# Optimization experiments

Measured on AMD Instinct MI355X. Metric: run time of the kernel, lower is better.

The kernel has to match this reference:

```python
import jax, jax.numpy as jnp
import numpy as np

BATCH, NODE, DIM = 4, 2048, 128
EPS = 1e-5


def _bn(x, gamma, beta):
    # BatchNorm1d in training mode: biased batch stats over rows, per-feature.
    mu = jnp.mean(x, axis=0)
    var = jnp.var(x, axis=0)
    return (x - mu) * jax.lax.rsqrt(var + EPS) * gamma + beta


def setup_inputs() -> dict:
    key = jax.random.key(0)
    ks = jax.random.split(key, 8)
    N = BATCH * NODE
    # Scale L like a normalized graph operator so activations stay sane.
    L = jax.random.normal(ks[0], (N, N), dtype=jnp.float32) / np.sqrt(N)
    inputs = jax.random.normal(ks[1], (BATCH, NODE, DIM), dtype=jnp.float32)
    mask = jnp.zeros((BATCH, NODE, 1), dtype=bool)  # unused in forward
    lim = 1.0 / np.sqrt(2 * DIM)
    fc0_w = jax.random.uniform(ks[2], (DIM, 2 * DIM), jnp.float32, -lim, lim)
    fc0_b = jax.random.uniform(ks[3], (DIM,), jnp.float32, -lim, lim)
    fc1_w = jax.random.uniform(ks[4], (DIM, 2 * DIM), jnp.float32, -lim, lim)
    fc1_b = jax.random.uniform(ks[5], (DIM,), jnp.float32, -lim, lim)
    bn0_gamma = jnp.ones((2 * DIM,), jnp.float32)
    bn0_beta = jnp.zeros((2 * DIM,), jnp.float32)
    bn1_gamma = jnp.ones((2 * DIM,), jnp.float32)
    bn1_beta = jnp.zeros((2 * DIM,), jnp.float32)
    return dict(L=L, mask=mask, inputs=inputs,
                bn0_gamma=bn0_gamma, bn0_beta=bn0_beta, fc0_w=fc0_w, fc0_b=fc0_b,
                bn1_gamma=bn1_gamma, bn1_beta=bn1_beta, fc1_w=fc1_w, fc1_b=fc1_b)


def reference(L, mask, inputs, bn0_gamma, bn0_beta, fc0_w, fc0_b,
              bn1_gamma, bn1_beta, fc1_w, fc1_b):
    b, n, d = inputs.shape

    def block(x, gamma, beta, w, bias):
        # x: (b, n, d). Laplacian propagation over flattened batch*node dim.
        xf = x.reshape(-1, d)                      # (b*n, d)
        Lx = (L @ xf).reshape(b, n, d)
        h = jnp.concatenate([x, Lx], axis=2).reshape(-1, 2 * d)
        h = _bn(h, gamma, beta)                    # pre-BN
        h = h @ w.T + bias                         # Linear(2d -> d)
        return h.reshape(b, n, d)

    x = jax.nn.elu(inputs)
    x = block(x, bn0_gamma, bn0_beta, fc0_w, fc0_b)
    x = jax.nn.elu(x)
    x = block(x, bn1_gamma, bn1_beta, fc1_w, fc1_b)
    return x + inputs
```

## Files before the change

### kernel.cpp

```cpp
#include <hip/hip_runtime.h>
#include <math.h>

#define NROWS 8192
#define DIM   128
#define FEAT  256
#define BK    128
#define NT    (NROWS / BK)

typedef __attribute__((ext_vector_type(8))) __bf16 bf16x8;
typedef __attribute__((ext_vector_type(8))) unsigned short u16x8;
typedef __attribute__((ext_vector_type(4))) unsigned short u16x4;
typedef __attribute__((ext_vector_type(4))) float f32x4;

__device__ __forceinline__ float bf2f(unsigned short h) {
  return __uint_as_float(((unsigned)h) << 16);
}
__device__ __forceinline__ unsigned short f2bf(float f) {
  unsigned u = __float_as_uint(f);
  return (unsigned short)((u + 0x7fff + ((u >> 16) & 1)) >> 16);
}
__device__ __forceinline__ void async16(const void* g, void* l) {
  __builtin_amdgcn_global_load_lds(
      (const __attribute__((address_space(1))) void*)g,
      (__attribute__((address_space(3))) void*)l, 16, 0, 0);
}
__device__ __forceinline__ f32x4 mfma16(bf16x8 a, bf16x8 b, f32x4 c) {
  return __builtin_amdgcn_mfma_f32_16x16x32_bf16(a, b, c, 0, 0, 0);
}
__device__ __forceinline__ float ldp(const void* p, int i, int is32) {
  return is32 ? ((const float*)p)[i] : bf2f(((const unsigned short*)p)[i]);
}

__global__ void detect_kernel(const unsigned short* __restrict__ L,
                              int* __restrict__ flag,
                              float* __restrict__ stats)
{
  for (int i = threadIdx.x; i < 1024; i += 256) stats[i] = 0.f;
  __shared__ int cnt;
  if (threadIdx.x == 0) cnt = 0;
  __syncthreads();
  int c = 0;
  for (int i = 0; i < 16; i++) {
    unsigned short s = L[2 * (threadIdx.x + 256 * i)];
    int e = (s >> 7) & 0xFF;
    if (e >= 192) c++;
  }
  atomicAdd(&cnt, c);
  __syncthreads();
  if (threadIdx.x == 0) *flag = (cnt > 16) ? 1 : 0;
}

__global__ __launch_bounds__(256) void trans_kernel(
    const void* __restrict__ src, unsigned short* __restrict__ xT,
    unsigned short* __restrict__ x0, unsigned short* __restrict__ inpc,
    float* __restrict__ stats, const int* __restrict__ flag)
{
  __shared__ __align__(16) unsigned short T[128 * 136];
  const int tid = threadIdx.x;
  const int r0 = blockIdx.x * 128;
  const int is32 = *flag;
  #pragma unroll
  for (int i = 0; i < 8; i++) {
    const int c = tid + 256 * i;
    const int rr = c >> 4, cg = c & 15;
    const size_t gidx = (size_t)(r0 + rr) * DIM + cg * 8;
    u16x8 v;
    if (is32) {
      const float* s = (const float*)src + gidx;
      f32x4 a = *(const f32x4*)s, b = *(const f32x4*)(s + 4);
      #pragma unroll
      for (int e = 0; e < 4; e++) { v[e] = f2bf(a[e]); v[e + 4] = f2bf(b[e]); }
    } else {
      v = *(const u16x8*)((const unsigned short*)src + gidx);
    }
    *(u16x8*)(inpc + gidx) = v;
    #pragma unroll
    for (int e = 0; e < 8; e++) {
      float f = bf2f(v[e]);
      f = f > 0.f ? f : expm1f(f);
      v[e] = f2bf(f);
    }
    *(u16x8*)(x0 + gidx) = v;
    *(u16x8*)(T + rr * 136 + cg * 8) = v;
  }
  __syncthreads();
  #pragma unroll
  for (int i = 0; i < 8; i++) {
    const int c = tid + 256 * i;
    const int n = c >> 4, mg = c & 15;
    u16x8 v;
    float s = 0.f, q = 0.f;
    #pragma unroll
    for (int e = 0; e < 8; e++) {
      unsigned short h = T[(mg * 8 + e) * 136 + n];
      v[e] = h;
      float f = bf2f(h);
      s += f; q += f * f;
    }
    *(u16x8*)(xT + (size_t)n * NROWS + r0 + mg * 8) = v;
    #pragma unroll
    for (int off = 1; off < 16; off <<= 1) {
      s += __shfl_xor(s, off, 16);
      q += __shfl_xor(q, off, 16);
    }
    if ((tid & 15) == 0) {
      atomicAdd(&stats[n], s);
      atomicAdd(&stats[256 + n], q);
    }
  }
}

template <int IS32>
__device__ __forceinline__ void gemm1_body(
    const void* __restrict__ Lraw, const unsigned short* __restrict__ xT,
    unsigned short* __restrict__ Lxb, float* __restrict__ stats,
    unsigned short* __restrict__ AsBase, unsigned short* __restrict__ BsBase)
{
  const int tid  = threadIdx.x;
  const int lane = tid & 63;
  const int wave = tid >> 6;
  const int wm = wave >> 2, wn = wave & 3;
  const int ln = lane & 15, quad = lane >> 4;
  const int m0 = blockIdx.x * 32;

  const int arow = tid >> 4, ap = tid & 15;
  const int akg = (ap & 8) | ((ap & 7) ^ (arow & 7));
  const float*          Lf = (const float*)Lraw;
  const unsigned short* Lh = (const unsigned short*)Lraw;
  const size_t Abase = (size_t)(m0 + arow) * NROWS + akg * 8;

  int brow[4], bkg[4];
  #pragma unroll
  for (int i = 0; i < 4; i++) {
    const int c = tid + (i << 9);
    brow[i] = c >> 4;
    const int p = c & 15;
    bkg[i] = (p & 8) | ((p & 7) ^ (brow[i] & 7));
  }

  unsigned short* a0 = AsBase;
  unsigned short* a1 = AsBase + 32 * 128;
  unsigned short* a2 = AsBase + 2 * 32 * 128;
  unsigned short* c0 = BsBase;
  unsigned short* c1 = BsBase + 128 * 128;
  unsigned short* c2 = BsBase + 2 * 128 * 128;

  f32x4 acc[2];
  acc[0] = (f32x4){0.f, 0.f, 0.f, 0.f};
  acc[1] = (f32x4){0.f, 0.f, 0.f, 0.f};

  auto issueB = [&](int kt, unsigned short* Bbuf) {
    const size_t koff = (size_t)kt * BK;
    #pragma unroll
    for (int i = 0; i < 4; i++) {
      const int c = tid + (i << 9);
      async16(xT + (size_t)brow[i] * NROWS + koff + bkg[i] * 8, Bbuf + c * 8);
    }
  };
  auto loadA = [&](int kt, f32x4& r0, f32x4& r1) {
    const float* s = Lf + Abase + (size_t)kt * BK;
    r0 = *(const f32x4*)s;
    r1 = *(const f32x4*)(s + 4);
  };
  auto issueA16 = [&](int kt, unsigned short* Abuf) {
    async16(Lh + Abase + (size_t)kt * BK, Abuf + arow * 128 + ap * 8);
  };
  auto writeA = [&](const f32x4& r0, const f32x4& r1, unsigned short* Abuf) {
    u16x8 o;
    #pragma unroll
    for (int e = 0; e < 4; e++) { o[e] = f2bf(r0[e]); o[e + 4] = f2bf(r1[e]); }
    *(u16x8*)(Abuf + arow * 128 + ap * 8) = o;
  };
  auto compute = [&](const unsigned short* Abuf, const unsigned short* Bbuf) {
    const int arf = wm * 16 + ln;
    const int brf = wn * 32 + ln;
    #pragma unroll
    for (int ks = 0; ks < 4; ks++) {
      const int kga = ks * 4 + quad;
      bf16x8 af = *(const bf16x8*)(Abuf + arf * 128 +
                     ((kga & 8) | ((kga & 7) ^ (arf & 7))) * 8);
      #pragma unroll
      for (int j = 0; j < 2; j++) {
        const int rb = brf + j * 16;
        bf16x8 bf = *(const bf16x8*)(Bbuf + rb * 128 +
                       ((kga & 8) | ((kga & 7) ^ (rb & 7))) * 8);
        acc[j] = mfma16(af, bf, acc[j]);
      }
    }
  };
  auto waitbar = [&]() {
    if (IS32) asm volatile("s_waitcnt vmcnt(6) lgkmcnt(0)" ::: "memory");
    else      asm volatile("s_waitcnt vmcnt(5) lgkmcnt(0)" ::: "memory");
    __builtin_amdgcn_s_barrier();
  };

  f32x4 e0, e1, o0, o1;

  issueB(0, c0);
  if (IS32) loadA(0, e0, e1); else issueA16(0, a0);
  issueB(1, c1);
  if (IS32) loadA(1, o0, o1); else issueA16(1, a1);
  if (IS32) writeA(e0, e1, a0);
  waitbar();

  for (int p = 0; p < 31; ++p) {
    const int t = 2 * p;
    issueB(t + 2, c2);
    if (IS32) loadA(t + 2, e0, e1); else issueA16(t + 2, a2);
    compute(a0, c0);
    if (IS32) writeA(o0, o1, a1);
    waitbar();
    issueB(t + 3, c0);
    if (IS32) loadA(t + 3, o0, o1); else issueA16(t + 3, a0);
    compute(a1, c1);
    if (IS32) writeA(e0, e1, a2);
    waitbar();
    unsigned short* tB = c2; c2 = c1; c1 = c0; c0 = tB;
    unsigned short* tA = a2; a2 = a1; a1 = a0; a0 = tA;
  }

  compute(a0, c0);
  if (IS32) writeA(o0, o1, a1);
  __syncthreads();
  compute(a1, c1);
  __syncthreads();

  float* E = (float*)AsBase;
  #pragma unroll
  for (int j = 0; j < 2; j++) {
    const int col = wn * 32 + j * 16 + ln;
    #pragma unroll
    for (int r = 0; r < 4; r++)
      E[(wm * 16 + quad * 4 + r) * 128 + col] = acc[j][r];
  }
  __syncthreads();
  {
    const int row = tid >> 4, cc0 = (tid & 15) * 8;
    u16x8 o;
    #pragma unroll
    for (int e = 0; e < 8; e++) o[e] = f2bf(E[row * 128 + cc0 + e]);
    *(u16x8*)(Lxb + (size_t)(m0 + row) * DIM + cc0) = o;
  }
  if (tid < 128) {
    float s = 0.f, q = 0.f;
    #pragma unroll
    for (int r = 0; r < 32; r++) {
      const float v = E[r * 128 + tid];
      s += v; q += v * v;
    }
    atomicAdd(&stats[128 + tid], s);
    atomicAdd(&stats[384 + tid], q);
  }
}

__global__ __launch_bounds__(512) void gemm1_fused(
    const void* __restrict__ Lraw, const unsigned short* __restrict__ xT,
    unsigned short* __restrict__ Lxb, float* __restrict__ stats,
    const int* __restrict__ flag)
{
  __shared__ __align__(16) unsigned short As[3 * 32 * 128];
  __shared__ __align__(16) unsigned short Bs[3 * 128 * 128];
  if (*flag) gemm1_body<1>(Lraw, xT, Lxb, stats, As, Bs);
  else       gemm1_body<0>(Lraw, xT, Lxb, stats, As, Bs);
}

__global__ void prep_kernel(const float* __restrict__ stats,
                            const void* __restrict__ gamma,
                            const void* __restrict__ beta,
                            const void* __restrict__ w,
                            const void* __restrict__ bias,
                            unsigned short* __restrict__ weff,
                            float* __restrict__ beff,
                            const int* __restrict__ flag)
{
  const int is32 = *flag;
  const int k = blockIdx.x;
  const int j = threadIdx.x;
  const float inv = 1.f / 8192.f;
  float mu = stats[j] * inv;
  float var = fmaxf(stats[256 + j] * inv - mu * mu, 0.f);
  float s = ldp(gamma, j, is32) * rsqrtf(var + 1e-5f);
  float wv = ldp(w, k * FEAT + j, is32);
  weff[(size_t)k * FEAT + j] = f2bf(wv * s);
  float term = (ldp(beta, j, is32) - mu * s) * wv;
  __shared__ float red[256];
  red[j] = term;
  __syncthreads();
  for (int off = 128; off > 0; off >>= 1) {
    if (j < off) red[j] += red[j + off];
    __syncthreads();
  }
  if (j == 0) beff[k] = ldp(bias, k, is32) + red[0];
}

__global__ __launch_bounds__(256) void gemm2_fc(
    const unsigned short* __restrict__ xb,
    const unsigned short* __restrict__ Lxb,
    const unsigned short* __restrict__ weff,
    const float* __restrict__ beff,
    const unsigned short* __restrict__ resid,
    void* __restrict__ outv,
    unsigned short* __restrict__ xTout,
    float* __restrict__ statsOut,
    int mode, const int* __restrict__ flag)
{
  __shared__ __align__(16) unsigned short As[32 * 264];
  const int is32 = *flag;
  const int tid = threadIdx.x;
  const int lane = tid & 63, wave = tid >> 6;
  const int m0 = blockIdx.x * 32;

  #pragma unroll
  for (int i = 0; i < 4; i++) {
    const int c = tid + 256 * i;
    const int mr = c >> 5, ch = c & 31;
    const unsigned short* src =
        (ch < 16) ? (xb  + (size_t)(m0 + mr) * DIM + ch * 8)
                  : (Lxb + (size_t)(m0 + mr) * DIM + (ch - 16) * 8);
    *(u16x8*)(As + mr * 264 + ch * 8) = *(const u16x8*)src;
  }
  __syncthreads();

  const int ln = lane & 15, quad = lane >> 4;
  const int nq = wave * 32;
  f32x4 acc[2][2];
  #pragma unroll
  for (int i = 0; i < 2; i++)
    #pragma unroll
    for (int j = 0; j < 2; j++)
      acc[i][j] = (f32x4){0.f, 0.f, 0.f, 0.f};

  #pragma unroll
  for (int ks = 0; ks < 8; ks++) {
    bf16x8 af[2], bfr[2];
    #pragma unroll
    for (int i = 0; i < 2; i++)
      af[i] = *(const bf16x8*)(As + (i * 16 + ln) * 264 + ks * 32 + quad * 8);
    #pragma unroll
    for (int j = 0; j < 2; j++)
      bfr[j] = *(const bf16x8*)(weff + (size_t)(nq + j * 16 + ln) * FEAT +
                                ks * 32 + quad * 8);
    #pragma unroll
    for (int i = 0; i < 2; i++)
      #pragma unroll
      for (int j = 0; j < 2; j++)
        acc[i][j] = mfma16(af[i], bfr[j], acc[i][j]);
  }

  #pragma unroll
  for (int j = 0; j < 2; j++) {
    const int gn = nq + j * 16 + ln;
    const float bb = beff[gn];
    float s = 0.f, q = 0.f;
    #pragma unroll
    for (int i = 0; i < 2; i++) {
      u16x4 pk;
      #pragma unroll
      for (int r = 0; r < 4; r++) {
        const int gm = m0 + i * 16 + quad * 4 + r;
        float v = acc[i][j][r] + bb;
        const size_t idx = (size_t)gm * DIM + gn;
        if (mode == 0) {
          v = v > 0.f ? v : expm1f(v);
          const unsigned short h = f2bf(v);
          ((unsigned short*)outv)[idx] = h;
          pk[r] = h;
          const float hv = bf2f(h);
          s += hv; q += hv * hv;
        } else {
          v += bf2f(resid[idx]);
          if (is32) ((float*)outv)[idx] = v;
          else      ((unsigned short*)outv)[idx] = f2bf(v);
        }
      }
      if (mode == 0)
        *(u16x4*)(xTout + (size_t)gn * NROWS + m0 + i * 16 + quad * 4) = pk;
    }
    if (mode == 0) {
      s += __shfl_xor(s, 16); q += __shfl_xor(q, 16);
      s += __shfl_xor(s, 32); q += __shfl_xor(q, 32);
      if (quad == 0) {
        atomicAdd(&statsOut[gn], s);
        atomicAdd(&statsOut[256 + gn], q);
      }
    }
  }
}

extern "C" void kernel_launch(void* const* d_in, const int* in_sizes, int n_in,
                              void* d_out, int out_size, void* d_ws, size_t ws_size,
                              hipStream_t stream) {
  const void* Lm   = d_in[0];
  const void* inp  = d_in[2];
  const void* bn0g = d_in[3];
  const void* bn0b = d_in[4];
  const void* fc0w = d_in[5];
  const void* fc0b = d_in[6];
  const void* bn1g = d_in[7];
  const void* bn1b = d_in[8];
  const void* fc1w = d_in[9];
  const void* fc1b = d_in[10];

  char* ws = (char*)d_ws;
  unsigned short* xT   = (unsigned short*)(ws);
  unsigned short* x0   = (unsigned short*)(ws + (2ull << 20));
  unsigned short* Lxb  = (unsigned short*)(ws + (4ull << 20));
  unsigned short* x1   = (unsigned short*)(ws + (6ull << 20));
  unsigned short* inpc = (unsigned short*)(ws + (8ull << 20));
  float*          stats= (float*)         (ws + (10ull << 20));
  int*            flag = (int*)           (ws + (10ull << 20) + 8192);
  float*          beff = (float*)         (ws + (10ull << 20) + 12288);
  unsigned short* weff = (unsigned short*)(ws + (10ull << 20) + 16384);

  detect_kernel<<<1, 256, 0, stream>>>((const unsigned short*)Lm, flag, stats);

  trans_kernel<<<64, 256, 0, stream>>>(inp, xT, x0, inpc, stats, flag);
  gemm1_fused<<<256, 512, 0, stream>>>(Lm, xT, Lxb, stats, flag);
  prep_kernel<<<128, 256, 0, stream>>>(stats, bn0g, bn0b, fc0w, fc0b,
                                       weff, beff, flag);
  gemm2_fc<<<256, 256, 0, stream>>>(x0, Lxb, weff, beff, nullptr, x1,
                                    xT, stats + 512, 0, flag);

  gemm1_fused<<<256, 512, 0, stream>>>(Lm, xT, Lxb, stats + 512, flag);
  prep_kernel<<<128, 256, 0, stream>>>(stats + 512, bn1g, bn1b, fc1w, fc1b,
                                       weff, beff, flag);
  gemm2_fc<<<256, 256, 0, stream>>>(x1, Lxb, weff, beff, inpc, d_out,
                                    nullptr, nullptr, 1, flag);
}
```

Baseline: 184.9 us.

## Restructure Laplacian GEMM to 16-row tiles with intra-block split-K across waves

The L@x GEMM kernel now uses 16-row output tiles with 256 threads and launches 512 blocks instead of 256. Each of the four waves computes the full 16x128 tile over its own quarter of each K-chunk, and the partial sums are reduced through LDS at the end. The triple-buffered pipeline with explicit vmcnt waits is replaced by a simpler double buffer synchronised with __syncthreads. The aim is more blocks per CU and more MFMA work per A fragment. In exchange, every block re-reads the full xT operand, so operand traffic doubles, and the load pipeline is shallower.

New measurement: 221.5 us. 19.8% more time.

```diff
diff --git a/kernel.cpp b/kernel.cpp
--- a/kernel.cpp
+++ b/kernel.cpp
@@ -118,10 +118,9 @@
 {
   const int tid  = threadIdx.x;
   const int lane = tid & 63;
-  const int wave = tid >> 6;
-  const int wm = wave >> 2, wn = wave & 3;
+  const int kq   = tid >> 6;
   const int ln = lane & 15, quad = lane >> 4;
-  const int m0 = blockIdx.x * 32;
+  const int m0 = blockIdx.x * 16;
 
   const int arow = tid >> 4, ap = tid & 15;
   const int akg = (ap & 8) | ((ap & 7) ^ (arow & 7));
@@ -129,31 +128,29 @@
   const unsigned short* Lh = (const unsigned short*)Lraw;
   const size_t Abase = (size_t)(m0 + arow) * NROWS + akg * 8;
 
-  int brow[4], bkg[4];
-  #pragma unroll
-  for (int i = 0; i < 4; i++) {
-    const int c = tid + (i << 9);
+  int brow[8], bkg[8];
+  #pragma unroll
+  for (int i = 0; i < 8; i++) {
+    const int c = tid + (i << 8);
     brow[i] = c >> 4;
     const int p = c & 15;
     bkg[i] = (p & 8) | ((p & 7) ^ (brow[i] & 7));
   }
 
-  unsigned short* a0 = AsBase;
-  unsigned short* a1 = AsBase + 32 * 128;
-  unsigned short* a2 = AsBase + 2 * 32 * 128;
-  unsigned short* c0 = BsBase;
-  unsigned short* c1 = BsBase + 128 * 128;
-  unsigned short* c2 = BsBase + 2 * 128 * 128;
-
-  f32x4 acc[2];
-  acc[0] = (f32x4){0.f, 0.f, 0.f, 0.f};
-  acc[1] = (f32x4){0.f, 0.f, 0.f, 0.f};
+  unsigned short* A0 = AsBase;
+  unsigned short* A1 = AsBase + 16 * 128;
+  unsigned short* B0 = BsBase;
+  unsigned short* B1 = BsBase + 128 * 128;
+
+  f32x4 acc[8];
+  #pragma unroll
+  for (int j = 0; j < 8; j++) acc[j] = (f32x4){0.f, 0.f, 0.f, 0.f};
 
   auto issueB = [&](int kt, unsigned short* Bbuf) {
     const size_t koff = (size_t)kt * BK;
     #pragma unroll
-    for (int i = 0; i < 4; i++) {
-      const int c = tid + (i << 9);
+    for (int i = 0; i < 8; i++) {
+      const int c = tid + (i << 8);
       async16(xT + (size_t)brow[i] * NROWS + koff + bkg[i] * 8, Bbuf + c * 8);
     }
   };
@@ -172,68 +169,52 @@
     *(u16x8*)(Abuf + arow * 128 + ap * 8) = o;
   };
   auto compute = [&](const unsigned short* Abuf, const unsigned short* Bbuf) {
-    const int arf = wm * 16 + ln;
-    const int brf = wn * 32 + ln;
-    #pragma unroll
-    for (int ks = 0; ks < 4; ks++) {
-      const int kga = ks * 4 + quad;
-      bf16x8 af = *(const bf16x8*)(Abuf + arf * 128 +
-                     ((kga & 8) | ((kga & 7) ^ (arf & 7))) * 8);
+    const int kga = kq * 4 + quad;
+    const int sw8 = ((kga & 8) | ((kga & 7) ^ (ln & 7))) * 8;
+    bf16x8 af = *(const bf16x8*)(Abuf + ln * 128 + sw8);
+    #pragma unroll
+    for (int nq = 0; nq < 8; nq++) {
+      bf16x8 bf = *(const bf16x8*)(Bbuf + (nq * 16 + ln) * 128 + sw8);
+      acc[nq] = mfma16(af, bf, acc[nq]);
+    }
+  };
+
+  issueB(0, B0);
+  f32x4 p0, p1;
+  if (IS32) { loadA(0, p0, p1); writeA(p0, p1, A0); }
+  else issueA16(0, A0);
+  __syncthreads();
+
+  unsigned short *Ac = A0, *An = A1, *Bc = B0, *Bn = B1;
+  for (int t = 0; t < NT; ++t) {
+    const bool more = (t + 1 < NT);
+    if (more) {
+      issueB(t + 1, Bn);
+      if (IS32) loadA(t + 1, p0, p1);
+      else      issueA16(t + 1, An);
+    }
+    compute(Ac, Bc);
+    if (IS32 && more) writeA(p0, p1, An);
+    __syncthreads();
+    unsigned short* x;
+    x = Ac; Ac = An; An = x;
+    x = Bc; Bc = Bn; Bn = x;
+  }
+
+  float* E = (float*)AsBase;
+  for (int g = 0; g < 4; g++) {
+    if (kq == g) {
       #pragma unroll
-      for (int j = 0; j < 2; j++) {
-        const int rb = brf + j * 16;
-        bf16x8 bf = *(const bf16x8*)(Bbuf + rb * 128 +
-                       ((kga & 8) | ((kga & 7) ^ (rb & 7))) * 8);
-        acc[j] = mfma16(af, bf, acc[j]);
-      }
-    }
-  };
-  auto waitbar = [&]() {
-    if (IS32) asm volatile("s_waitcnt vmcnt(6) lgkmcnt(0)" ::: "memory");
-    else      asm volatile("s_waitcnt vmcnt(5) lgkmcnt(0)" ::: "memory");
-    __builtin_amdgcn_s_barrier();
-  };
-
-  f32x4 e0, e1, o0, o1;
-
-  issueB(0, c0);
-  if (IS32) loadA(0, e0, e1); else issueA16(0, a0);
-  issueB(1, c1);
-  if (IS32) loadA(1, o0, o1); else issueA16(1, a1);
-  if (IS32) writeA(e0, e1, a0);
-  waitbar();
-
-  for (int p = 0; p < 31; ++p) {
-    const int t = 2 * p;
-    issueB(t + 2, c2);
-    if (IS32) loadA(t + 2, e0, e1); else issueA16(t + 2, a2);
-    compute(a0, c0);
-    if (IS32) writeA(o0, o1, a1);
-    waitbar();
-    issueB(t + 3, c0);
-    if (IS32) loadA(t + 3, o0, o1); else issueA16(t + 3, a0);
-    compute(a1, c1);
-    if (IS32) writeA(e0, e1, a2);
-    waitbar();
-    unsigned short* tB = c2; c2 = c1; c1 = c0; c0 = tB;
-    unsigned short* tA = a2; a2 = a1; a1 = a0; a0 = tA;
-  }
-
-  compute(a0, c0);
-  if (IS32) writeA(o0, o1, a1);
-  __syncthreads();
-  compute(a1, c1);
-  __syncthreads();
-
-  float* E = (float*)AsBase;
-  #pragma unroll
-  for (int j = 0; j < 2; j++) {
-    const int col = wn * 32 + j * 16 + ln;
-    #pragma unroll
-    for (int r = 0; r < 4; r++)
-      E[(wm * 16 + quad * 4 + r) * 128 + col] = acc[j][r];
-  }
-  __syncthreads();
+      for (int nq = 0; nq < 8; nq++)
+        #pragma unroll
+        for (int r = 0; r < 4; r++) {
+          float* p = &E[(quad * 4 + r) * 128 + nq * 16 + ln];
+          if (g == 0) *p = acc[nq][r];
+          else        *p += acc[nq][r];
+        }
+    }
+    __syncthreads();
+  }
   {
     const int row = tid >> 4, cc0 = (tid & 15) * 8;
     u16x8 o;
@@ -244,7 +225,7 @@
   if (tid < 128) {
     float s = 0.f, q = 0.f;
     #pragma unroll
-    for (int r = 0; r < 32; r++) {
+    for (int r = 0; r < 16; r++) {
       const float v = E[r * 128 + tid];
       s += v; q += v * v;
     }
@@ -253,13 +234,13 @@
   }
 }
 
-__global__ __launch_bounds__(512) void gemm1_fused(
+__global__ __launch_bounds__(256) void gemm1_fused(
     const void* __restrict__ Lraw, const unsigned short* __restrict__ xT,
     unsigned short* __restrict__ Lxb, float* __restrict__ stats,
     const int* __restrict__ flag)
 {
-  __shared__ __align__(16) unsigned short As[3 * 32 * 128];
-  __shared__ __align__(16) unsigned short Bs[3 * 128 * 128];
+  __shared__ __align__(16) unsigned short As[2 * 16 * 128];
+  __shared__ __align__(16) unsigned short Bs[2 * 128 * 128];
   if (*flag) gemm1_body<1>(Lraw, xT, Lxb, stats, As, Bs);
   else       gemm1_body<0>(Lraw, xT, Lxb, stats, As, Bs);
 }
@@ -415,13 +396,13 @@
   detect_kernel<<<1, 256, 0, stream>>>((const unsigned short*)Lm, flag, stats);
 
   trans_kernel<<<64, 256, 0, stream>>>(inp, xT, x0, inpc, stats, flag);
-  gemm1_fused<<<256, 512, 0, stream>>>(Lm, xT, Lxb, stats, flag);
+  gemm1_fused<<<512, 256, 0, stream>>>(Lm, xT, Lxb, stats, flag);
   prep_kernel<<<128, 256, 0, stream>>>(stats, bn0g, bn0b, fc0w, fc0b,
                                        weff, beff, flag);
   gemm2_fc<<<256, 256, 0, stream>>>(x0, Lxb, weff, beff, nullptr, x1,
                                     xT, stats + 512, 0, flag);
 
-  gemm1_fused<<<256, 512, 0, stream>>>(Lm, xT, Lxb, stats + 512, flag);
+  gemm1_fused<<<512, 256, 0, stream>>>(Lm, xT, Lxb, stats + 512, flag);
   prep_kernel<<<128, 256, 0, stream>>>(stats + 512, bn1g, bn1b, fc1w, fc1b,
                                        weff, beff, flag);
   gemm2_fc<<<256, 256, 0, stream>>>(x1, Lxb, weff, beff, inpc, d_out,
```
